# Performance work log

Measured on AMD Instinct MI355X. Metric: run time of the kernel, lower is better.

## Reference

```python
import jax, jax.numpy as jnp
import numpy as np

N = 50000   # nodes
E = 800000  # edges (avg degree 16)
H = 128     # hidden_dim / emb_dim
OUT = 128   # out_dim
NUM_BOND_TYPE = 6
NUM_BOND_DIR = 6


def setup_inputs() -> dict:
    key = jax.random.key(0)
    ks = jax.random.split(key, 12)
    s = 0.05
    return {
        "x": jax.random.normal(ks[0], (N, H), jnp.float32),
        "edge_index": jax.random.randint(ks[1], (2, E), 0, N),
        "edge_attr": jax.random.randint(ks[2], (E, 2), 0, 6),
        "prelu_a": jnp.float32(0.25),  # PReLU single shared slope (torch default)
        "W_enc": jax.random.normal(ks[3], (H, H), jnp.float32) * s,  # enc_to_dec, no bias
        "edge_emb1": jax.random.normal(ks[4], (NUM_BOND_TYPE, H), jnp.float32) * s,
        "edge_emb2": jax.random.normal(ks[5], (NUM_BOND_DIR, H), jnp.float32) * s,
        "W1": jax.random.normal(ks[6], (H, 2 * H), jnp.float32) * s,
        "b1": jnp.zeros((2 * H,), jnp.float32),
        "W2": jax.random.normal(ks[7], (2 * H, OUT), jnp.float32) * s,
        "b2": jnp.zeros((OUT,), jnp.float32),
    }


def reference(x, edge_index, edge_attr, prelu_a, W_enc, edge_emb1, edge_emb2, W1, b1, W2, b2):
    n = x.shape[0]
    # GNNDecoder: PReLU then enc_to_dec linear (no bias)
    x = jnp.where(x > 0, x, prelu_a * x)
    x = x @ W_enc

    # GINConv.forward: add self loops, self-loop edge_attr = [5, 0]
    loop = jnp.arange(n)
    src = jnp.concatenate([edge_index[0], loop])  # [E+N]
    dst = jnp.concatenate([edge_index[1], loop])  # [E+N]
    ea1 = jnp.concatenate([edge_attr[:, 0], jnp.full((n,), 5, edge_attr.dtype)])
    ea2 = jnp.concatenate([edge_attr[:, 1], jnp.zeros((n,), edge_attr.dtype)])

    # edge embedding lookup + gather-add message + scatter-add aggregate
    edge_emb = edge_emb1[ea1] + edge_emb2[ea2]          # [E+N, H]
    msg = x[src] + edge_emb                             # message(x_j, edge_attr)
    agg = jax.ops.segment_sum(msg, dst, num_segments=n)  # aggr='add'

    # update: MLP Linear(H,2H) -> SiLU -> Linear(2H,OUT)
    h = jax.nn.silu(agg @ W1 + b1)
    return h @ W2 + b2
```

## Files before the change

kernel.cpp:

```cpp
#include <hip/hip_runtime.h>

typedef unsigned short u16;
typedef unsigned int   u32;
typedef __attribute__((ext_vector_type(8))) short short8;
typedef __attribute__((ext_vector_type(4))) float f32x4;

#define MAXDEG 64

__device__ __forceinline__ float bl(u32 u){ union{u32 i; float f;} c; c.i = u << 16; return c.f; }
__device__ __forceinline__ float bh(u32 u){ union{u32 i; float f;} c; c.i = u & 0xffff0000u; return c.f; }
__device__ __forceinline__ u16 f2b(float f){
  union{float f; u32 i;} c; c.f = f;
  return (u16)((c.i + 0x8000u) >> 16);
}
__device__ __forceinline__ u32 pk2(float a, float b){
  union{float f; u32 i;} x, y; x.f = a; y.f = b;
  return ((x.i + 0x8000u) >> 16) | ((y.i + 0x8000u) & 0xffff0000u);
}

__device__ __forceinline__ void tr_tile(
    const float* __restrict__ in, int K, int Nn, u16* __restrict__ out,
    int k0, int n0, int t, u16* __restrict__ sT )
{
  #pragma unroll
  for (int rr = 0; rr < 4; rr++) {
    int row = (t >> 4) + rr * 16;
    int c4  = (t & 15) * 4;
    float4 v = *(const float4*)&in[(size_t)(k0 + row) * Nn + n0 + c4];
    sT[(c4 + 0) * 72 + row] = f2b(v.x);
    sT[(c4 + 1) * 72 + row] = f2b(v.y);
    sT[(c4 + 2) * 72 + row] = f2b(v.z);
    sT[(c4 + 3) * 72 + row] = f2b(v.w);
  }
  __syncthreads();
  #pragma unroll
  for (int ww = 0; ww < 2; ww++) {
    int nn = (t >> 3) + ww * 32;
    int c8 = (t & 7) * 8;
    uint4 val = *(const uint4*)&sT[nn * 72 + c8];
    *(uint4*)&out[(size_t)(n0 + nn) * K + k0 + c8] = val;
  }
}

__global__ __launch_bounds__(256) void k_prep(
    const float* __restrict__ Wenc, const float* __restrict__ W1,
    const float* __restrict__ W2, const float* __restrict__ e1,
    const float* __restrict__ e2, u16* __restrict__ WencT,
    u16* __restrict__ W1T, u16* __restrict__ W2T,
    u32* __restrict__ embP, int* __restrict__ cnt, int N)
{
  __shared__ u16 sT[64 * 72];
  const int b = blockIdx.x, t = threadIdx.x;

  if (b < 4) {
    tr_tile(Wenc, 128, 128, WencT, (b & 1) * 64, (b >> 1) * 64, t, sT);
  } else if (b < 12) {
    int l = b - 4;
    tr_tile(W1, 128, 256, W1T, (l & 1) * 64, (l >> 1) * 64, t, sT);
  } else if (b < 20) {
    int l = b - 12;
    tr_tile(W2, 256, 128, W2T, (l & 3) * 64, (l >> 2) * 64, t, sT);
  } else if (b == 20) {
    for (int i = t; i < 2304; i += 256) {
      int q = i / 576, rem = i - q * 576;
      int c = rem >> 4, s = rem & 15;
      int c1 = c / 6, c2 = c - c1 * 6;
      int col = q * 32 + s * 2;
      embP[i] = pk2(e1[c1 * 128 + col]     + e2[c2 * 128 + col],
                    e1[c1 * 128 + col + 1] + e2[c2 * 128 + col + 1]);
    }
  } else {
    int base = (b - 21) * 1024 + t * 4;
    if (base + 3 < N) *(int4*)&cnt[base] = make_int4(0, 0, 0, 0);
    else {
      if (base     < N) cnt[base]     = 0;
      if (base + 1 < N) cnt[base + 1] = 0;
      if (base + 2 < N) cnt[base + 2] = 0;
      if (base + 3 < N) cnt[base + 3] = 0;
    }
  }
}

__global__ __launch_bounds__(256) void k_enc_count(
    const float* __restrict__ x, const float* __restrict__ pa,
    const u16* __restrict__ WT, u16* __restrict__ xencQ, int N,
    const int* __restrict__ ei, const int* __restrict__ ea,
    int* __restrict__ cnt, u32* __restrict__ recs,
    int E, int encBlocks)
{
  if ((int)blockIdx.x >= encBlocks) {
    int e = ((int)blockIdx.x - encBlocks) * 256 + threadIdx.x;
    if (e < E) {
      int src = ei[e];
      int dst = ei[E + e];
      int2 a = *(const int2*)&ea[2 * e];
      int r = atomicAdd(&cnt[dst], 1);
      if (r < MAXDEG)
        recs[(size_t)dst * MAXDEG + r] =
            (u32)src | ((u32)(a.x * 6 + a.y) << 26);
    }
    return;
  }

  const int SK = 136, NT = 8;
  __shared__ u16 sB[128 * SK];

  const int t = threadIdx.x;
  #pragma unroll
  for (int j = 0; j < 8; j++) {
    int i = t + 256 * j;
    int n = i >> 4, k8 = i & 15;
    *(uint4*)&sB[n * SK + k8 * 8] = *(const uint4*)&WT[n * 128 + k8 * 8];
  }
  __syncthreads();

  const float slope = pa[0];
  const int lane = t & 63, wave = t >> 6, quad = lane >> 4, l16 = lane & 15;
  const int m0 = blockIdx.x * 128 + wave * 32;
  if (m0 >= N) return;

  f32x4 acc[2][NT];
  #pragma unroll
  for (int mr = 0; mr < 2; mr++)
    #pragma unroll
    for (int nt = 0; nt < NT; nt++) acc[mr][nt] = (f32x4){0.f, 0.f, 0.f, 0.f};

  #pragma unroll
  for (int ks = 0; ks < 4; ks++) {
    const int k0 = ks * 32 + quad * 8;
    union { u32 u[4]; short8 s; } a[2];
    #pragma unroll
    for (int mr = 0; mr < 2; mr++) {
      int row = m0 + mr * 16 + l16; row = min(row, N - 1);
      const float4* ap = (const float4*)&x[(size_t)row * 128 + k0];
      float4 f0 = ap[0], f1 = ap[1];
      float v0 = f0.x > 0.f ? f0.x : slope * f0.x;
      float v1 = f0.y > 0.f ? f0.y : slope * f0.y;
      float v2 = f0.z > 0.f ? f0.z : slope * f0.z;
      float v3 = f0.w > 0.f ? f0.w : slope * f0.w;
      float v4 = f1.x > 0.f ? f1.x : slope * f1.x;
      float v5 = f1.y > 0.f ? f1.y : slope * f1.y;
      float v6 = f1.z > 0.f ? f1.z : slope * f1.z;
      float v7 = f1.w > 0.f ? f1.w : slope * f1.w;
      a[mr].u[0] = pk2(v0, v1); a[mr].u[1] = pk2(v2, v3);
      a[mr].u[2] = pk2(v4, v5); a[mr].u[3] = pk2(v6, v7);
    }
    #pragma unroll
    for (int nt = 0; nt < NT; nt++) {
      short8 b = *(const short8*)&sB[(nt * 16 + l16) * SK + k0];
      acc[0][nt] = __builtin_amdgcn_mfma_f32_16x16x32_bf16(a[0].s, b, acc[0][nt], 0, 0, 0);
      acc[1][nt] = __builtin_amdgcn_mfma_f32_16x16x32_bf16(a[1].s, b, acc[1][nt], 0, 0, 0);
    }
  }

  #pragma unroll
  for (int mr = 0; mr < 2; mr++)
    #pragma unroll
    for (int nt = 0; nt < NT; nt++) {
      int col = nt * 16 + l16;
      int q = col >> 5, cq = col & 31;
      #pragma unroll
      for (int r = 0; r < 4; r++) {
        int row = m0 + mr * 16 + quad * 4 + r;
        if (row < N)
          xencQ[((size_t)q * N + row) * 32 + cq] = f2b(acc[mr][nt][r]);
      }
    }
}

struct B8 { uint2 x[8]; u32 r[8]; };

__device__ __forceinline__ void issue8(B8& b, u32 rv, int grp,
                                       const u32* __restrict__ xq, int sub) {
  #pragma unroll
  for (int k = 0; k < 8; k++) {
    u32 r = __shfl(rv, grp + k);
    b.r[k] = r;
    b.x[k] = *(const uint2*)&xq[(size_t)(r & 0x3ffffffu) * 16 + sub * 2];
  }
}

__device__ __forceinline__ void acc8(float* a, const B8& b,
                                     const u32* __restrict__ sEq,
                                     int sub, int dleft) {
  #pragma unroll
  for (int k = 0; k < 8; k++) {
    if (k < dleft) {
      uint2 e = *(const uint2*)&sEq[(b.r[k] >> 26) * 18 + sub * 2];
      uint2 x = b.x[k];
      a[0] += bl(x.x) + bl(e.x);  a[1] += bh(x.x) + bh(e.x);
      a[2] += bl(x.y) + bl(e.y);  a[3] += bh(x.y) + bh(e.y);
    }
  }
}

__global__ __launch_bounds__(256) void k_gather(
    const int* __restrict__ cnt, const u32* __restrict__ recs,
    const u32* __restrict__ embP, const u32* __restrict__ xencQ,
    u32* __restrict__ aggbQ, int N, int nodeBlocks)
{
  const int ES = 18;
  __shared__ u32 sE[36 * ES];

  const int t = threadIdx.x;
  const int q = (int)blockIdx.x / nodeBlocks;
  const int nbid = (int)blockIdx.x - q * nodeBlocks;

  for (int i = t; i < 576; i += 256) {
    int c = i >> 4, s = i & 15;
    sE[c * ES + s] = embP[q * 576 + i];
  }
  __syncthreads();

  const int lane = t & 63, wave = t >> 6;
  const int grp = lane & 56, sub = lane & 7;
  const int v = nbid * 32 + wave * 8 + (lane >> 3);
  const bool vok = v < N;
  const int vc = vok ? v : N - 1;
  const int d = vok ? min(cnt[vc], MAXDEG) : 0;
  const int beg = vc * MAXDEG;
  const int end = beg + d;

  u32 rv0 = 0, rv1 = 0, rv2 = 0, rv3 = 0;
  if (d > 0)  rv0 = recs[min(beg + sub, end - 1)];
  if (d > 8)  rv1 = recs[min(beg + 8 + sub, end - 1)];
  if (d > 16) rv2 = recs[min(beg + 16 + sub, end - 1)];
  if (d > 24) rv3 = recs[min(beg + 24 + sub, end - 1)];

  const u32* xq = xencQ + (size_t)q * N * 16;

  uint2 xs = *(const uint2*)&xq[(size_t)vc * 16 + sub * 2];
  uint2 es = *(const uint2*)&sE[30 * ES + sub * 2];
  float a[4];
  a[0] = bl(xs.x) + bl(es.x);  a[1] = bh(xs.x) + bh(es.x);
  a[2] = bl(xs.y) + bl(es.y);  a[3] = bh(xs.y) + bh(es.y);

  if (d > 0) {
    B8 bA, bB;
    issue8(bA, rv0, grp, xq, sub);
    if (d > 8) issue8(bB, rv1, grp, xq, sub);
    acc8(a, bA, sE, sub, d);
    if (d > 8) {
      if (d > 16) issue8(bA, rv2, grp, xq, sub);
      acc8(a, bB, sE, sub, d - 8);
      if (d > 16) {
        if (d > 24) issue8(bB, rv3, grp, xq, sub);
        acc8(a, bA, sE, sub, d - 16);
        if (d > 24) {
          acc8(a, bB, sE, sub, d - 24);
          for (int j0 = 32; j0 < d; j0 += 8) {
            u32 rvt = recs[min(beg + j0 + sub, end - 1)];
            issue8(bA, rvt, grp, xq, sub);
            acc8(a, bA, sE, sub, d - j0);
          }
        }
      }
    }
  }

  if (vok) {
    uint2 o;
    o.x = pk2(a[0], a[1]);
    o.y = pk2(a[2], a[3]);
    *(uint2*)&aggbQ[((size_t)q * N + vc) * 16 + sub * 2] = o;
  }
}

__global__ __launch_bounds__(256) void k_mlp(
    const u16* __restrict__ aggbQ, const u16* __restrict__ W1T,
    const float* __restrict__ b1, const u16* __restrict__ W2T,
    const float* __restrict__ b2, float* __restrict__ out, int N)
{
  const int SK = 136;
  __shared__ u16 sW[128 * SK];
  __shared__ u16 sH[128 * SK];
  __shared__ float sB1[256];
  __shared__ float sB2[128];

  const int t = threadIdx.x;
  const int lane = t & 63, wave = t >> 6, quad = lane >> 4, l16 = lane & 15;
  const int m0 = blockIdx.x * 128 + wave * 32;

  if (t < 128) sB2[t] = b2[t];
  sB1[t] = b1[t];

  union { uint4 q; short8 s; } a[2][4];
  #pragma unroll
  for (int mr = 0; mr < 2; mr++) {
    int row = min(m0 + mr * 16 + l16, N - 1);
    #pragma unroll
    for (int ks = 0; ks < 4; ks++)
      a[mr][ks].q = *(const uint4*)&aggbQ[((size_t)ks * N + row) * 32 + quad * 8];
  }

  f32x4 acc2[2][8];
  #pragma unroll
  for (int mr = 0; mr < 2; mr++)
    #pragma unroll
    for (int nt = 0; nt < 8; nt++) acc2[mr][nt] = (f32x4){0.f, 0.f, 0.f, 0.f};

  for (int half = 0; half < 2; half++) {
    #pragma unroll
    for (int j = 0; j < 8; j++) {
      int i = t + 256 * j;
      int n = i >> 4, k8 = i & 15;
      *(uint4*)&sW[n * SK + k8 * 8] =
          *(const uint4*)&W1T[(size_t)(half * 128 + n) * 128 + k8 * 8];
    }
    __syncthreads();

    f32x4 acc1[2][8];
    #pragma unroll
    for (int mr = 0; mr < 2; mr++)
      #pragma unroll
      for (int nt = 0; nt < 8; nt++) acc1[mr][nt] = (f32x4){0.f, 0.f, 0.f, 0.f};

    #pragma unroll
    for (int ks = 0; ks < 4; ks++) {
      const int k0 = ks * 32 + quad * 8;
      #pragma unroll
      for (int nt = 0; nt < 8; nt++) {
        short8 b = *(const short8*)&sW[(nt * 16 + l16) * SK + k0];
        acc1[0][nt] = __builtin_amdgcn_mfma_f32_16x16x32_bf16(a[0][ks].s, b, acc1[0][nt], 0, 0, 0);
        acc1[1][nt] = __builtin_amdgcn_mfma_f32_16x16x32_bf16(a[1][ks].s, b, acc1[1][nt], 0, 0, 0);
      }
    }

    #pragma unroll
    for (int mr = 0; mr < 2; mr++)
      #pragma unroll
      for (int nt = 0; nt < 8; nt++) {
        int col = nt * 16 + l16;
        float bias = sB1[half * 128 + col];
        #pragma unroll
        for (int r = 0; r < 4; r++) {
          float z = acc1[mr][nt][r] + bias;
          float s = z / (1.f + __expf(-z));
          sH[(wave * 32 + mr * 16 + quad * 4 + r) * SK + col] = f2b(s);
        }
      }
    __syncthreads();

    #pragma unroll
    for (int j = 0; j < 8; j++) {
      int i = t + 256 * j;
      int n = i >> 4, k8 = i & 15;
      *(uint4*)&sW[n * SK + k8 * 8] =
          *(const uint4*)&W2T[(size_t)n * 256 + half * 128 + k8 * 8];
    }
    __syncthreads();

    #pragma unroll
    for (int ks = 0; ks < 4; ks++) {
      const int k0 = ks * 32 + quad * 8;
      union { uint4 q; short8 s; } ah[2];
      #pragma unroll
      for (int mr = 0; mr < 2; mr++)
        ah[mr].q = *(const uint4*)&sH[(wave * 32 + mr * 16 + l16) * SK + k0];
      #pragma unroll
      for (int nt = 0; nt < 8; nt++) {
        short8 b = *(const short8*)&sW[(nt * 16 + l16) * SK + k0];
        acc2[0][nt] = __builtin_amdgcn_mfma_f32_16x16x32_bf16(ah[0].s, b, acc2[0][nt], 0, 0, 0);
        acc2[1][nt] = __builtin_amdgcn_mfma_f32_16x16x32_bf16(ah[1].s, b, acc2[1][nt], 0, 0, 0);
      }
    }
    __syncthreads();
  }

  #pragma unroll
  for (int mr = 0; mr < 2; mr++)
    #pragma unroll
    for (int nt = 0; nt < 8; nt++) {
      int col = nt * 16 + l16;
      float bias = sB2[col];
      #pragma unroll
      for (int r = 0; r < 4; r++) {
        int row = m0 + mr * 16 + quad * 4 + r;
        if (row < N) out[(size_t)row * 128 + col] = acc2[mr][nt][r] + bias;
      }
    }
}

extern "C" void kernel_launch(void* const* d_in, const int* in_sizes, int n_in,
                              void* d_out, int out_size, void* d_ws, size_t ws_size,
                              hipStream_t stream) {
  const float* x    = (const float*)d_in[0];
  const int*   ei   = (const int*)d_in[1];
  const int*   ea   = (const int*)d_in[2];
  const float* pa   = (const float*)d_in[3];
  const float* Wenc = (const float*)d_in[4];
  const float* e1   = (const float*)d_in[5];
  const float* e2   = (const float*)d_in[6];
  const float* W1   = (const float*)d_in[7];
  const float* b1   = (const float*)d_in[8];
  const float* W2   = (const float*)d_in[9];
  const float* b2   = (const float*)d_in[10];
  float* out = (float*)d_out;

  const int N = in_sizes[0] / 128;
  const int E = in_sizes[1] / 2;

  char* ws = (char*)d_ws;
  size_t off = 0;
  auto alloc = [&](size_t bytes) {
    void* p = ws + off;
    off = (off + bytes + 255) & ~(size_t)255;
    return p;
  };
  u16*   xencQ  = (u16*)  alloc((size_t)N * 128 * 2);
  u32*   aggbQ  = (u32*)  alloc((size_t)N * 64 * 4);
  int*   cnt    = (int*)  alloc((size_t)N * 4);
  u32*   recs   = (u32*)  alloc((size_t)N * MAXDEG * 4);
  u16*   WencT  = (u16*)  alloc(128 * 128 * 2);
  u16*   W1T    = (u16*)  alloc(256 * 128 * 2);
  u16*   W2T    = (u16*)  alloc(128 * 256 * 2);
  u32*   embP   = (u32*)  alloc(2304 * 4);

  const int encBlocks   = (N + 127) / 128;
  const int edgeBlocks  = (E + 255) / 256;
  const int nodeBlocks  = (N + 31) / 32;
  const int prepBlocks  = 21 + (N + 1023) / 1024;

  k_prep<<<prepBlocks, 256, 0, stream>>>(Wenc, W1, W2, e1, e2,
                                         WencT, W1T, W2T, embP, cnt, N);
  k_enc_count<<<encBlocks + edgeBlocks, 256, 0, stream>>>(
      x, pa, WencT, xencQ, N, ei, ea, cnt, recs, E, encBlocks);
  k_gather<<<4 * nodeBlocks, 256, 0, stream>>>(
      cnt, recs, embP, (const u32*)xencQ, aggbQ, N, nodeBlocks);
  k_mlp<<<encBlocks, 256, 0, stream>>>(
      (const u16*)aggbQ, W1T, b1, W2T, b2, out, N);
}
```

Measured before the change: 204.4 us.

## Replace global atomic edge scatter with two-pass bucketed binning through LDS

Edge records are no longer placed with one global atomicAdd per edge into per-destination slots. Each edge block first bins its 2048 edges into 256-node buckets using LDS atomics and writes them to a per-block staging area. A new k_place kernel then reads, per bucket, every block's entries and assigns per-node slots with LDS atomics, writing the node counts directly, so the counter-zeroing pass is dropped from k_prep. This trades contended random global atomics for an extra kernel launch, a large staging buffer, and a fixed per-bucket cap of 40 that would silently drop edges if exceeded.

New measurement: 209.1 us. 2.3% more time.

```diff
diff --git a/kernel.cpp b/kernel.cpp
--- a/kernel.cpp
+++ b/kernel.cpp
@@ -6,6 +6,8 @@
 typedef __attribute__((ext_vector_type(4))) float f32x4;
 
 #define MAXDEG 64
+#define CAP    40
+#define EB     2048
 
 __device__ __forceinline__ float bl(u32 u){ union{u32 i; float f;} c; c.i = u << 16; return c.f; }
 __device__ __forceinline__ float bh(u32 u){ union{u32 i; float f;} c; c.i = u & 0xffff0000u; return c.f; }
@@ -47,7 +49,7 @@
     const float* __restrict__ W2, const float* __restrict__ e1,
     const float* __restrict__ e2, u16* __restrict__ WencT,
     u16* __restrict__ W1T, u16* __restrict__ W2T,
-    u32* __restrict__ embP, int* __restrict__ cnt, int N)
+    u32* __restrict__ embP)
 {
   __shared__ u16 sT[64 * 72];
   const int b = blockIdx.x, t = threadIdx.x;
@@ -60,7 +62,7 @@
   } else if (b < 20) {
     int l = b - 12;
     tr_tile(W2, 256, 128, W2T, (l & 3) * 64, (l >> 2) * 64, t, sT);
-  } else if (b == 20) {
+  } else {
     for (int i = t; i < 2304; i += 256) {
       int q = i / 576, rem = i - q * 576;
       int c = rem >> 4, s = rem & 15;
@@ -69,15 +71,6 @@
       embP[i] = pk2(e1[c1 * 128 + col]     + e2[c2 * 128 + col],
                     e1[c1 * 128 + col + 1] + e2[c2 * 128 + col + 1]);
     }
-  } else {
-    int base = (b - 21) * 1024 + t * 4;
-    if (base + 3 < N) *(int4*)&cnt[base] = make_int4(0, 0, 0, 0);
-    else {
-      if (base     < N) cnt[base]     = 0;
-      if (base + 1 < N) cnt[base + 1] = 0;
-      if (base + 2 < N) cnt[base + 2] = 0;
-      if (base + 3 < N) cnt[base + 3] = 0;
-    }
   }
 }
 
@@ -85,20 +78,43 @@
     const float* __restrict__ x, const float* __restrict__ pa,
     const u16* __restrict__ WT, u16* __restrict__ xencQ, int N,
     const int* __restrict__ ei, const int* __restrict__ ea,
-    int* __restrict__ cnt, u32* __restrict__ recs,
-    int E, int encBlocks)
+    uint2* __restrict__ binned, int* __restrict__ bcnt,
+    int E, int encBlocks, int nBuckets)
 {
   if ((int)blockIdx.x >= encBlocks) {
-    int e = ((int)blockIdx.x - encBlocks) * 256 + threadIdx.x;
-    if (e < E) {
-      int src = ei[e];
-      int dst = ei[E + e];
-      int2 a = *(const int2*)&ea[2 * e];
-      int r = atomicAdd(&cnt[dst], 1);
-      if (r < MAXDEG)
-        recs[(size_t)dst * MAXDEG + r] =
-            (u32)src | ((u32)(a.x * 6 + a.y) << 26);
-    }
+    __shared__ int cntB[256];
+    const int t = threadIdx.x;
+    const int blk = (int)blockIdx.x - encBlocks;
+    cntB[t] = 0;
+    __syncthreads();
+
+    const int e0 = blk * EB;
+    u32 recx[8]; int bkt[8], nl[8]; bool ok[8];
+    #pragma unroll
+    for (int j = 0; j < 8; j++) {
+      int e = e0 + 256 * j + t;
+      ok[j] = e < E;
+      if (ok[j]) {
+        int src = ei[e];
+        int dst = ei[E + e];
+        int2 a = *(const int2*)&ea[2 * e];
+        recx[j] = (u32)src | ((u32)(a.x * 6 + a.y) << 26);
+        bkt[j] = dst >> 8;
+        nl[j]  = dst & 255;
+      }
+    }
+    uint2* myRegion = binned + (size_t)blk * nBuckets * CAP;
+    #pragma unroll
+    for (int j = 0; j < 8; j++) {
+      if (ok[j]) {
+        int slot = atomicAdd(&cntB[bkt[j]], 1);
+        if (slot < CAP)
+          myRegion[bkt[j] * CAP + slot] = make_uint2(recx[j], (u32)nl[j]);
+      }
+    }
+    __syncthreads();
+    for (int i = t; i < nBuckets; i += 256)
+      bcnt[blk * nBuckets + i] = min(cntB[i], CAP);
     return;
   }
 
@@ -166,6 +182,37 @@
           xencQ[((size_t)q * N + row) * 32 + cq] = f2b(acc[mr][nt][r]);
       }
     }
+}
+
+__global__ __launch_bounds__(256) void k_place(
+    const uint2* __restrict__ binned, const int* __restrict__ bcnt,
+    u32* __restrict__ recs, int* __restrict__ cnt,
+    int N, int nBlkA, int nBuckets)
+{
+  __shared__ int cntL[256];
+  __shared__ int sBC[512];
+  const int b = blockIdx.x, t = threadIdx.x;
+
+  cntL[t] = 0;
+  const int nA = min(nBlkA, 512);
+  for (int i = t; i < nA; i += 256) sBC[i] = bcnt[i * nBuckets + b];
+  __syncthreads();
+
+  const int total = nA * CAP;
+  for (int i = t; i < total; i += 256) {
+    int blk = i / CAP, j = i - blk * CAP;
+    if (j < sBC[blk]) {
+      uint2 r = binned[((size_t)blk * nBuckets + b) * CAP + j];
+      int nl = (int)r.y;
+      int slot = atomicAdd(&cntL[nl], 1);
+      if (slot < MAXDEG)
+        recs[(size_t)((b << 8) + nl) * MAXDEG + slot] = r.x;
+    }
+  }
+  __syncthreads();
+
+  int node = (b << 8) + t;
+  if (node < N) cnt[node] = min(cntL[t], MAXDEG);
 }
 
 struct B8 { uint2 x[8]; u32 r[8]; };
@@ -400,6 +447,11 @@
   const int N = in_sizes[0] / 128;
   const int E = in_sizes[1] / 2;
 
+  const int encBlocks = (N + 127) / 128;
+  const int nBlkA     = (E + EB - 1) / EB;
+  const int nBuckets  = (N + 255) / 256;
+  const int nodeBlocks = (N + 31) / 32;
+
   char* ws = (char*)d_ws;
   size_t off = 0;
   auto alloc = [&](size_t bytes) {
@@ -409,22 +461,21 @@
   };
   u16*   xencQ  = (u16*)  alloc((size_t)N * 128 * 2);
   u32*   aggbQ  = (u32*)  alloc((size_t)N * 64 * 4);
-  int*   cnt    = (int*)  alloc((size_t)N * 4);
-  u32*   recs   = (u32*)  alloc((size_t)N * MAXDEG * 4);
+  int*   cnt    = (int*)  alloc((size_t)nBuckets * 256 * 4);
+  u32*   recs   = (u32*)  alloc((size_t)nBuckets * 256 * MAXDEG * 4);
+  uint2* binned = (uint2*)alloc((size_t)nBlkA * nBuckets * CAP * 8);
+  int*   bcnt   = (int*)  alloc((size_t)nBlkA * nBuckets * 4);
   u16*   WencT  = (u16*)  alloc(128 * 128 * 2);
   u16*   W1T    = (u16*)  alloc(256 * 128 * 2);
   u16*   W2T    = (u16*)  alloc(128 * 256 * 2);
   u32*   embP   = (u32*)  alloc(2304 * 4);
 
-  const int encBlocks   = (N + 127) / 128;
-  const int edgeBlocks  = (E + 255) / 256;
-  const int nodeBlocks  = (N + 31) / 32;
-  const int prepBlocks  = 21 + (N + 1023) / 1024;
-
-  k_prep<<<prepBlocks, 256, 0, stream>>>(Wenc, W1, W2, e1, e2,
-                                         WencT, W1T, W2T, embP, cnt, N);
-  k_enc_count<<<encBlocks + edgeBlocks, 256, 0, stream>>>(
-      x, pa, WencT, xencQ, N, ei, ea, cnt, recs, E, encBlocks);
+  k_prep<<<21, 256, 0, stream>>>(Wenc, W1, W2, e1, e2,
+                                 WencT, W1T, W2T, embP);
+  k_enc_count<<<encBlocks + nBlkA, 256, 0, stream>>>(
+      x, pa, WencT, xencQ, N, ei, ea, binned, bcnt, E, encBlocks, nBuckets);
+  k_place<<<nBuckets, 256, 0, stream>>>(
+      binned, bcnt, recs, cnt, N, nBlkA, nBuckets);
   k_gather<<<4 * nodeBlocks, 256, 0, stream>>>(
       cnt, recs, embP, (const u32*)xencQ, aggbQ, N, nodeBlocks);
   k_mlp<<<encBlocks, 256, 0, stream>>>(
```
